# Optimization experiments

Hardware: AMD Instinct MI355X
Metric: run time of the kernel (lower is better)

Reference implementation:

```python
import jax, jax.numpy as jnp
import numpy as np

# constants mirroring init_kwargs
SPATIAL_STRIDE = 4
RADIUS2 = 0.5 ** 2
K = 32


def _fps(xyz, m):
    """Iterative farthest point sampling. xyz: [N,3] -> idx [m] int32 (starts at index 0, like pointnet2)."""
    n = xyz.shape[0]

    def body(i, carry):
        dist, idx = carry
        cur = xyz[idx[i]]                              # [3]
        d = jnp.sum((xyz - cur) ** 2, axis=-1)          # [N]
        dist = jnp.minimum(dist, d)
        idx = idx.at[i + 1].set(jnp.argmax(dist).astype(jnp.int32))
        return dist, idx

    dist0 = jnp.full((n,), 1e10, xyz.dtype)
    idx0 = jnp.zeros((m,), jnp.int32)
    _, idx = jax.lax.fori_loop(0, m - 1, body, (dist0, idx0))
    return idx


def setup_inputs() -> dict:
    key = jax.random.key(0)
    ks = jax.random.split(key, 5)
    B, T, N, C = 4, 8, 2048, 64
    C_IN = 2 * C + 3  # grouped feat2 + anchor feat1 + xyz displacement
    xyzs = jax.random.uniform(ks[0], (B, T, N, 3), dtype=jnp.float32)
    features = jax.random.normal(ks[1], (B, T, N, C), dtype=jnp.float32)
    w1 = jax.random.normal(ks[2], (C_IN, 128), dtype=jnp.float32) / np.sqrt(C_IN)
    w2 = jax.random.normal(ks[3], (128, 128), dtype=jnp.float32) / np.sqrt(128)
    w3 = jax.random.normal(ks[4], (128, 256), dtype=jnp.float32) / np.sqrt(128)
    return {
        "xyzs": xyzs, "features": features,
        "w1": w1, "b1": jnp.zeros((128,), jnp.float32),
        "w2": w2, "b2": jnp.zeros((128,), jnp.float32),
        "w3": w3, "b3": jnp.zeros((256,), jnp.float32),
    }


def reference(xyzs, features, w1, b1, w2, b2, w3, b3):
    B, T, N, _ = xyzs.shape
    M = N // SPATIAL_STRIDE

    # temporal replicate padding [1,1]
    xp = jnp.concatenate([xyzs[:, :1], xyzs, xyzs[:, -1:]], axis=1)        # [B,T+2,N,3]
    fp = jnp.concatenate([features[:, :1], features, features[:, -1:]], axis=1)
    # frames processed: i = 1..T (stride 1); neighbor frame = i+1
    xyz_a, xyz_n = xp[:, 1:T + 1], xp[:, 2:T + 2]                          # [B,T,N,3]
    feat_a, feat_n = fp[:, 1:T + 1], fp[:, 2:T + 2]                        # [B,T,N,C]

    gather = jax.vmap(jax.vmap(lambda a, i: a[i]))  # over (B, T)

    # FPS on each anchor frame
    idx = jax.vmap(jax.vmap(lambda p: _fps(p, M)))(xyz_a)                  # [B,T,M]
    anchor = gather(xyz_a, idx)                                            # [B,T,M,3]
    f1 = gather(feat_a, idx)                                               # [B,T,M,C]

    # knn of anchors into next frame, with ball-query radius clamp
    d = jnp.sum((anchor[:, :, :, None, :] - xyz_n[:, :, None, :, :]) ** 2, axis=-1)  # [B,T,M,N]
    negd, idxk = jax.lax.top_k(-d, K)                                      # [B,T,M,K]
    idxk = jnp.where(-negd <= RADIUS2, idxk, idxk[..., :1])                # duplicate nearest outside radius

    gxyz = gather(xyz_n, idxk)                                             # [B,T,M,K,3]
    gf2 = gather(feat_n, idxk)                                             # [B,T,M,K,C]
    disp = gxyz - anchor[:, :, :, None, :]
    h = jnp.concatenate(
        [gf2, jnp.broadcast_to(f1[:, :, :, None, :], gf2.shape), disp], axis=-1)  # [B,T,M,K,2C+3]

    h = jax.nn.relu(h @ w1 + b1)
    h = jax.nn.relu(h @ w2 + b2)
    h = jax.nn.relu(h @ w3 + b3)
    new_features = jnp.max(h, axis=3)                                      # [B,T,M,256]
    return anchor, new_features
```

## Files before the change

### kernel.cpp

```cpp
#include <hip/hip_runtime.h>

#define BB 4
#define TT 8
#define NN 2048
#define CC 64
#define MM 512
#define KK 32
#define H3DIM 256
#define RAD2 0.25f
#define FINF 3.4e38f

typedef _Float16 f16x8 __attribute__((ext_vector_type(8)));
typedef _Float16 f16x4 __attribute__((ext_vector_type(4)));
typedef float f32x4 __attribute__((ext_vector_type(4)));

template <int CTRL>
__device__ __forceinline__ float dpp_max_step(float x) {
    int xi = __builtin_bit_cast(int, x);
    int yi = __builtin_amdgcn_update_dpp(xi, xi, CTRL, 0xf, 0xf, false);
    return fmaxf(x, __builtin_bit_cast(float, yi));
}
__device__ __forceinline__ float wave_max64(float x) {
    x = dpp_max_step<0x111>(x);
    x = dpp_max_step<0x112>(x);
    x = dpp_max_step<0x114>(x);
    x = dpp_max_step<0x118>(x);
    x = dpp_max_step<0x142>(x);
    x = dpp_max_step<0x143>(x);
    return __builtin_bit_cast(float, __builtin_amdgcn_readlane(__builtin_bit_cast(int, x), 63));
}
template <int CTRL>
__device__ __forceinline__ float dpp_min_step(float x) {
    int xi = __builtin_bit_cast(int, x);
    int yi = __builtin_amdgcn_update_dpp(xi, xi, CTRL, 0xf, 0xf, false);
    return fminf(x, __builtin_bit_cast(float, yi));
}
__device__ __forceinline__ float wave_minf64(float x) {
    x = dpp_min_step<0x111>(x);
    x = dpp_min_step<0x112>(x);
    x = dpp_min_step<0x114>(x);
    x = dpp_min_step<0x118>(x);
    x = dpp_min_step<0x142>(x);
    x = dpp_min_step<0x143>(x);
    return __builtin_bit_cast(float, __builtin_amdgcn_readlane(__builtin_bit_cast(int, x), 63));
}
template <int CTRL>
__device__ __forceinline__ int dpp_imin_step(int x) {
    int yi = __builtin_amdgcn_update_dpp(x, x, CTRL, 0xf, 0xf, false);
    return (yi < x) ? yi : x;
}
__device__ __forceinline__ int wave_mini64(int x) {
    x = dpp_imin_step<0x111>(x);
    x = dpp_imin_step<0x112>(x);
    x = dpp_imin_step<0x114>(x);
    x = dpp_imin_step<0x118>(x);
    x = dpp_imin_step<0x142>(x);
    x = dpp_imin_step<0x143>(x);
    return __builtin_amdgcn_readlane(x, 63);
}

__global__ __launch_bounds__(256) void k_fps(const float* __restrict__ xyzs,
                                             int* __restrict__ fps_idx) {
    int bt = blockIdx.x;
    int tid = threadIdx.x;
    int lane = tid & 63, w = tid >> 6;
    __shared__ float sx[NN], sy[NN], sz[NN];
    __shared__ float pd[2][4];
    __shared__ int   pi[2][4];
    const float* src = xyzs + (size_t)bt * NN * 3;
    for (int i = tid; i < NN; i += 256) {
        sx[i] = src[i * 3 + 0];
        sy[i] = src[i * 3 + 1];
        sz[i] = src[i * 3 + 2];
    }
    __syncthreads();

    float px[8], py[8], pz[8], dist[8];
#pragma unroll
    for (int j = 0; j < 8; ++j) {
        int p = tid * 8 + j;
        px[j] = sx[p]; py[j] = sy[p]; pz[j] = sz[p];
        dist[j] = 1e10f;
    }

    int cur = 0;
    if (tid == 0) fps_idx[bt * MM + 0] = 0;
    int pbase = tid * 8;

    for (int it = 1; it < MM; ++it) {
        float cx = sx[cur], cy = sy[cur], cz = sz[cur];
        float bestd = -1.0f;
        int bestp = 0;
#pragma unroll
        for (int j = 0; j < 8; ++j) {
            float dx = px[j] - cx, dy = py[j] - cy, dz = pz[j] - cz;
            float d = dx * dx + dy * dy + dz * dz;
            float nd = fminf(dist[j], d);
            dist[j] = nd;
            if (nd > bestd) { bestd = nd; bestp = pbase + j; }
        }
        float wmax = wave_max64(bestd);
        unsigned long long mask = __ballot(bestd == wmax);
        int wl = __ffsll(mask) - 1;
        int wbp = __builtin_amdgcn_readlane(bestp, wl);
        if (lane == 0) { pd[it & 1][w] = wmax; pi[it & 1][w] = wbp; }
        __syncthreads();
        float bd = pd[it & 1][0];
        int bp = pi[it & 1][0];
#pragma unroll
        for (int q = 1; q < 4; ++q) {
            float d2 = pd[it & 1][q];
            int p2 = pi[it & 1][q];
            if (d2 > bd) { bd = d2; bp = p2; }
        }
        cur = bp;
        if (tid == 0) fps_idx[bt * MM + it] = cur;
    }
}

__global__ __launch_bounds__(256) void k_pp(const float* __restrict__ xyzs,
                                            const float* __restrict__ feats,
                                            const float* __restrict__ w1,
                                            _Float16* __restrict__ Pp) {
    __shared__ float sw[68 * 128];
    __shared__ float sin_[64 * 68];
    int tid = threadIdx.x;
    for (int i = tid; i < 68 * 128; i += 256) {
        int r = i >> 7, c = i & 127;
        float v = 0.f;
        if (r < 64) v = w1[r * 128 + c];
        else if (r < 67) v = w1[(128 + r - 64) * 128 + c];
        sw[i] = v;
    }
    int row0 = blockIdx.x * 64;
    int bt = row0 >> 11;
    int b = bt >> 3, t = bt & 7;
    int tn = (t + 1 < TT) ? (t + 1) : (TT - 1);
    size_t nbase = (size_t)(b * TT + tn) * NN + (row0 & (NN - 1));
    const float* fsrc = feats + nbase * CC;
    const float* xsrc = xyzs + nbase * 3;
    for (int i = tid; i < 1024; i += 256) {
        float4 v = ((const float4*)fsrc)[i];
        int r = i >> 4, c = (i & 15) * 4;
        *(float4*)&sin_[r * 68 + c] = v;
    }
    if (tid < 192) {
        int r = tid / 3, c = tid - r * 3;
        sin_[r * 68 + 64 + c] = xsrc[tid];
    }
    if (tid < 64) sin_[tid * 68 + 67] = 0.f;
    __syncthreads();

    int rowg = tid >> 5, colg = tid & 31;
    float4 acc[8];
#pragma unroll
    for (int i = 0; i < 8; ++i) acc[i] = make_float4(0.f, 0.f, 0.f, 0.f);
    for (int k = 0; k < 68; k += 4) {
        float4 a4[8], b4[4];
#pragma unroll
        for (int i = 0; i < 8; ++i) a4[i] = *(const float4*)&sin_[(rowg * 8 + i) * 68 + k];
#pragma unroll
        for (int kk = 0; kk < 4; ++kk) b4[kk] = *(const float4*)&sw[(k + kk) * 128 + colg * 4];
#pragma unroll
        for (int i = 0; i < 8; ++i) {
#pragma unroll
            for (int kk = 0; kk < 4; ++kk) {
                float av = (kk == 0) ? a4[i].x : (kk == 1) ? a4[i].y : (kk == 2) ? a4[i].z : a4[i].w;
                acc[i].x += av * b4[kk].x;
                acc[i].y += av * b4[kk].y;
                acc[i].z += av * b4[kk].z;
                acc[i].w += av * b4[kk].w;
            }
        }
    }
#pragma unroll
    for (int i = 0; i < 8; ++i) {
        f16x4 h;
        h[0] = (_Float16)acc[i].x; h[1] = (_Float16)acc[i].y;
        h[2] = (_Float16)acc[i].z; h[3] = (_Float16)acc[i].w;
        *(f16x4*)&Pp[(size_t)(row0 + rowg * 8 + i) * 128 + colg * 4] = h;
    }
}

__global__ __launch_bounds__(256) void k_qp(const float* __restrict__ xyzs,
                                            const float* __restrict__ feats,
                                            const float* __restrict__ w1,
                                            const float* __restrict__ b1,
                                            const int* __restrict__ fps_idx,
                                            float* __restrict__ Qp,
                                            float* __restrict__ out_anchor) {
    __shared__ float sw[68 * 128];
    __shared__ float sin_[64 * 68];
    __shared__ float sb[128];
    int tid = threadIdx.x;
    for (int i = tid; i < 68 * 128; i += 256) {
        int r = i >> 7, c = i & 127;
        float v = 0.f;
        if (r < 64) v = w1[(64 + r) * 128 + c];
        else if (r < 67) v = w1[(128 + r - 64) * 128 + c];
        sw[i] = v;
    }
    if (tid < 128) sb[tid] = b1[tid];
    int row0 = blockIdx.x * 64;
    int bt = row0 >> 9;
    size_t fbase = (size_t)bt * NN;
    {
        int r = tid >> 2, seg = tid & 3;
        int aidx = fps_idx[row0 + r];
        const float4* fr = (const float4*)(feats + (fbase + aidx) * CC);
#pragma unroll
        for (int i = 0; i < 4; ++i) {
            float4 v = fr[seg * 4 + i];
            *(float4*)&sin_[r * 68 + seg * 16 + i * 4] = v;
        }
    }
    if (tid < 64) {
        int aidx = fps_idx[row0 + tid];
        const float* xs = xyzs + (fbase + aidx) * 3;
        float x = xs[0], y = xs[1], z = xs[2];
        sin_[tid * 68 + 64] = -x;
        sin_[tid * 68 + 65] = -y;
        sin_[tid * 68 + 66] = -z;
        sin_[tid * 68 + 67] = 0.f;
        out_anchor[(size_t)(row0 + tid) * 3 + 0] = x;
        out_anchor[(size_t)(row0 + tid) * 3 + 1] = y;
        out_anchor[(size_t)(row0 + tid) * 3 + 2] = z;
    }
    __syncthreads();

    int rowg = tid >> 5, colg = tid & 31;
    float4 bias = *(const float4*)&sb[colg * 4];
    float4 acc[8];
#pragma unroll
    for (int i = 0; i < 8; ++i) acc[i] = bias;
    for (int k = 0; k < 68; k += 4) {
        float4 a4[8], b4[4];
#pragma unroll
        for (int i = 0; i < 8; ++i) a4[i] = *(const float4*)&sin_[(rowg * 8 + i) * 68 + k];
#pragma unroll
        for (int kk = 0; kk < 4; ++kk) b4[kk] = *(const float4*)&sw[(k + kk) * 128 + colg * 4];
#pragma unroll
        for (int i = 0; i < 8; ++i) {
#pragma unroll
            for (int kk = 0; kk < 4; ++kk) {
                float av = (kk == 0) ? a4[i].x : (kk == 1) ? a4[i].y : (kk == 2) ? a4[i].z : a4[i].w;
                acc[i].x += av * b4[kk].x;
                acc[i].y += av * b4[kk].y;
                acc[i].z += av * b4[kk].z;
                acc[i].w += av * b4[kk].w;
            }
        }
    }
#pragma unroll
    for (int i = 0; i < 8; ++i)
        *(float4*)&Qp[(size_t)(row0 + rowg * 8 + i) * 128 + colg * 4] = acc[i];
}

__global__ __launch_bounds__(256) void k_knn(const float* __restrict__ xyzs,
                                             const float* __restrict__ anchors,
                                             int* __restrict__ idxk) {
    __shared__ float sx[NN], sy[NN], sz[NN];
    int tid = threadIdx.x;
    int wave = tid >> 6, lane = tid & 63;
    int bt = blockIdx.x >> 6;
    int sub = blockIdx.x & 63;
    int b = bt >> 3, t = bt & 7;
    int tn = (t + 1 < TT) ? (t + 1) : (TT - 1);
    const float* src = xyzs + ((size_t)(b * TT + tn)) * NN * 3;
    for (int i = tid; i < NN; i += 256) {
        sx[i] = src[i * 3 + 0];
        sy[i] = src[i * 3 + 1];
        sz[i] = src[i * 3 + 2];
    }
    __syncthreads();

    for (int a = 0; a < 2; ++a) {
        int mrow = bt * MM + sub * 8 + wave * 2 + a;
        float ax = anchors[mrow * 3 + 0];
        float ay = anchors[mrow * 3 + 1];
        float az = anchors[mrow * 3 + 2];
        float d[32];
#pragma unroll
        for (int j = 0; j < 32; ++j) {
            int p = j * 64 + lane;
            float dx = sx[p] - ax, dy = sy[p] - ay, dz = sz[p] - az;
            d[j] = dx * dx + dy * dy + dz * dz;
        }
        float bd = FINF;
        int bp = 0x7fffffff;
#pragma unroll
        for (int j = 0; j < 32; ++j) {
            if (d[j] < bd) { bd = d[j]; bp = j * 64 + lane; }
        }
        float wmin = wave_minf64(bd);
        int cand = (bd == wmin) ? bp : 0x7fffffff;
        int gp = wave_mini64(cand);
        int p0 = gp;
        int myidx = gp;
        int pstar = gp;

        for (int r = 1; r < KK; ++r) {
            bd = FINF;
            bp = 0x7fffffff;
#pragma unroll
            for (int j = 0; j < 32; ++j) {
                int pj = j * 64 + lane;
                float dj = (pj == pstar) ? FINF : d[j];
                d[j] = dj;
                if (dj < bd) { bd = dj; bp = pj; }
            }
            wmin = wave_minf64(bd);
            cand = (bd == wmin) ? bp : 0x7fffffff;
            gp = wave_mini64(cand);
            int outp = (wmin <= RAD2) ? gp : p0;
            if (lane == r) myidx = outp;
            pstar = gp;
        }
        if (lane < KK) idxk[(size_t)mrow * KK + lane] = myidx;
    }
}

#define SM_W2 0
#define SM_W3 32768
#define SM_H1 98304
#define SM_H2 114688
#define SM_B2 131072
#define SM_B3 131584
#define SM_TOTAL 132608

__global__ __launch_bounds__(512, 1) void k_mlp(const _Float16* __restrict__ Pp,
                                                const float* __restrict__ Qp,
                                                const int* __restrict__ idxk,
                                                const float* __restrict__ w2,
                                                const float* __restrict__ b2,
                                                const float* __restrict__ w3,
                                                const float* __restrict__ b3,
                                                float* __restrict__ out_feat) {
    extern __shared__ char smem[];
    int tid = threadIdx.x;
    int bid = blockIdx.x;

    for (int i = tid; i < 128 * 128; i += 512) {
        int n = i & 127, kk = i >> 7;
        _Float16 v = (_Float16)w2[kk * 128 + n];
        *(_Float16*)(smem + SM_W2 + n * 256 + ((2 * kk) ^ ((n & 7) << 4))) = v;
    }
    for (int i = tid; i < 256 * 128; i += 512) {
        int n = i & 255, kk = i >> 8;
        _Float16 v = (_Float16)w3[kk * 256 + n];
        *(_Float16*)(smem + SM_W3 + n * 256 + ((2 * kk) ^ ((n & 7) << 4))) = v;
    }
    if (tid < 128) *(float*)(smem + SM_B2 + tid * 4) = b2[tid];
    if (tid < 256) *(float*)(smem + SM_B3 + tid * 4) = b3[tid];
    __syncthreads();

    int lane = tid & 63;
    int w = tid >> 6;
    int wm = w >> 2, wn = w & 3;
    int l15 = lane & 15, g = lane >> 4;
    int hswz = (l15 & 7) << 4;

    const f32x4 zero4 = {0.f, 0.f, 0.f, 0.f};

    for (int c = 0; c < 32; ++c) {
        int a0 = bid * 64 + c * 2;
        int bt = a0 >> 9;

        {
            int r = tid >> 3, seg = tid & 7;
            int arow = a0 + (r >> 5);
            int kidx = r & 31;
            int nk = idxk[(size_t)arow * KK + kidx];
            const _Float16* ps = Pp + ((size_t)(bt * NN + nk)) * 128 + seg * 16;
            const float* qs = Qp + (size_t)arow * 128 + seg * 16;
            int rowbase = SM_H1 + r * 256;
            int swz = (r & 7) << 4;
#pragma unroll
            for (int i = 0; i < 2; ++i) {
                f16x8 pv = *(const f16x8*)(ps + i * 8);
                f32x4 q0 = *(const f32x4*)(qs + i * 8);
                f32x4 q1 = *(const f32x4*)(qs + i * 8 + 4);
                f16x8 hv;
#pragma unroll
                for (int j = 0; j < 4; ++j) hv[j] = (_Float16)fmaxf((float)pv[j] + q0[j], 0.f);
#pragma unroll
                for (int j = 0; j < 4; ++j) hv[4 + j] = (_Float16)fmaxf((float)pv[4 + j] + q1[j], 0.f);
                *(f16x8*)(smem + rowbase + ((seg * 32 + i * 16) ^ swz)) = hv;
            }
        }
        __syncthreads();

        f32x4 acc2[2][2];
#pragma unroll
        for (int m = 0; m < 2; ++m)
#pragma unroll
            for (int n = 0; n < 2; ++n) acc2[m][n] = zero4;

#pragma unroll
        for (int ks = 0; ks < 4; ++ks) {
            int kbyte = ks * 64 + g * 16;
            f16x8 af[2], bf[2];
#pragma unroll
            for (int m = 0; m < 2; ++m) {
                int row = wm * 32 + m * 16 + l15;
                af[m] = *(const f16x8*)(smem + SM_H1 + row * 256 + (kbyte ^ hswz));
            }
#pragma unroll
            for (int n = 0; n < 2; ++n) {
                int col = wn * 32 + n * 16 + l15;
                bf[n] = *(const f16x8*)(smem + SM_W2 + col * 256 + (kbyte ^ hswz));
            }
#pragma unroll
            for (int m = 0; m < 2; ++m)
#pragma unroll
                for (int n = 0; n < 2; ++n)
                    acc2[m][n] = __builtin_amdgcn_mfma_f32_16x16x32_f16(af[m], bf[n], acc2[m][n], 0, 0, 0);
        }
#pragma unroll
        for (int m = 0; m < 2; ++m)
#pragma unroll
            for (int n = 0; n < 2; ++n) {
                int col = wn * 32 + n * 16 + l15;
                float bb = *(const float*)(smem + SM_B2 + col * 4);
#pragma unroll
                for (int r = 0; r < 4; ++r) {
                    int row = wm * 32 + m * 16 + g * 4 + r;
                    float v = fmaxf(acc2[m][n][r] + bb, 0.f);
                    *(_Float16*)(smem + SM_H2 + row * 256 + ((2 * col) ^ ((row & 7) << 4))) = (_Float16)v;
                }
            }
        __syncthreads();

        f32x4 acc3[2][4];
#pragma unroll
        for (int m = 0; m < 2; ++m)
#pragma unroll
            for (int n = 0; n < 4; ++n) acc3[m][n] = zero4;

#pragma unroll
        for (int ks = 0; ks < 4; ++ks) {
            int kbyte = ks * 64 + g * 16;
            f16x8 af[2], bf[4];
#pragma unroll
            for (int m = 0; m < 2; ++m) {
                int row = wm * 32 + m * 16 + l15;
                af[m] = *(const f16x8*)(smem + SM_H2 + row * 256 + (kbyte ^ hswz));
            }
#pragma unroll
            for (int n = 0; n < 4; ++n) {
                int col = wn * 64 + n * 16 + l15;
                bf[n] = *(const f16x8*)(smem + SM_W3 + col * 256 + (kbyte ^ hswz));
            }
#pragma unroll
            for (int m = 0; m < 2; ++m)
#pragma unroll
                for (int n = 0; n < 4; ++n)
                    acc3[m][n] = __builtin_amdgcn_mfma_f32_16x16x32_f16(af[m], bf[n], acc3[m][n], 0, 0, 0);
        }
#pragma unroll
        for (int n = 0; n < 4; ++n) {
            int col = wn * 64 + n * 16 + l15;
            float s = acc3[0][n][0];
#pragma unroll
            for (int r = 1; r < 4; ++r) s = fmaxf(s, acc3[0][n][r]);
#pragma unroll
            for (int r = 0; r < 4; ++r) s = fmaxf(s, acc3[1][n][r]);
            s = fmaxf(s, __shfl_xor(s, 16));
            s = fmaxf(s, __shfl_xor(s, 32));
            if (g == 0) {
                float bb = *(const float*)(smem + SM_B3 + col * 4);
                out_feat[(size_t)(a0 + wm) * H3DIM + col] = fmaxf(s + bb, 0.f);
            }
        }
        __syncthreads();
    }
}

extern "C" void kernel_launch(void* const* d_in, const int* in_sizes, int n_in,
                              void* d_out, int out_size, void* d_ws, size_t ws_size,
                              hipStream_t stream) {
    const float* xyzs  = (const float*)d_in[0];
    const float* feats = (const float*)d_in[1];
    const float* w1 = (const float*)d_in[2];
    const float* b1 = (const float*)d_in[3];
    const float* w2 = (const float*)d_in[4];
    const float* b2 = (const float*)d_in[5];
    const float* w3 = (const float*)d_in[6];
    const float* b3 = (const float*)d_in[7];

    float* out_anchor = (float*)d_out;
    float* out_feat = out_anchor + (size_t)BB * TT * MM * 3;

    char* ws = (char*)d_ws;
    int* fps_idx = (int*)ws;
    int* idxk = (int*)(ws + 65536);
    _Float16* Pp = (_Float16*)(ws + 65536 + 2097152);
    float* Qp = (float*)(ws + 65536 + 2097152 + 16777216);
    if (ws_size < (size_t)(65536 + 2097152 + 16777216) + (size_t)BB * TT * MM * 128 * 4)
        return;

    k_fps<<<BB * TT, 256, 0, stream>>>(xyzs, fps_idx);
    k_pp<<<BB * TT * NN / 64, 256, 0, stream>>>(xyzs, feats, w1, Pp);
    k_qp<<<BB * TT * MM / 64, 256, 0, stream>>>(xyzs, feats, w1, b1, fps_idx, Qp, out_anchor);
    k_knn<<<BB * TT * 64, 256, 0, stream>>>(xyzs, out_anchor, idxk);

    (void)hipFuncSetAttribute((const void*)k_mlp, hipFuncAttributeMaxDynamicSharedMemorySize, SM_TOTAL);
    k_mlp<<<256, 512, SM_TOTAL, stream>>>(Pp, Qp, idxk, w2, b2, w3, b3, out_feat);
}
```

Before: 595.8 us.

## Pack distance and index into 64-bit keys for single-pass wave argmax/argmin

FPS and kNN reductions now pack the float distance and point index into one 64-bit key, so a single DPP reduction finds both the extreme value and the winning index. This replaces the separate max, ballot and readlane sequence, or the min-value then min-index pair of reductions. In FPS the winning wave writes the winner's coordinates into shared memory alongside the key, which removes the dependent LDS read of the next centroid on the serial critical path. In kNN the per-lane scan becomes a tree of four groups, and only the winning lane's slot is invalidated, which shortens the dependency chain. The cost is that each DPP step moves two 32-bit halves and does a 64-bit compare; tie-breaking relies on the non-negative float bit patterns ordering the same way as the floats.

```diff
diff --git a/kernel.cpp b/kernel.cpp
--- a/kernel.cpp
+++ b/kernel.cpp
@@ -15,58 +15,53 @@
 typedef float f32x4 __attribute__((ext_vector_type(4)));
 
 template <int CTRL>
-__device__ __forceinline__ float dpp_max_step(float x) {
-    int xi = __builtin_bit_cast(int, x);
-    int yi = __builtin_amdgcn_update_dpp(xi, xi, CTRL, 0xf, 0xf, false);
-    return fmaxf(x, __builtin_bit_cast(float, yi));
-}
-__device__ __forceinline__ float wave_max64(float x) {
-    x = dpp_max_step<0x111>(x);
-    x = dpp_max_step<0x112>(x);
-    x = dpp_max_step<0x114>(x);
-    x = dpp_max_step<0x118>(x);
-    x = dpp_max_step<0x142>(x);
-    x = dpp_max_step<0x143>(x);
-    return __builtin_bit_cast(float, __builtin_amdgcn_readlane(__builtin_bit_cast(int, x), 63));
+__device__ __forceinline__ unsigned long long dpp_maxkey_step(unsigned long long k) {
+    int lo = (int)(unsigned)k;
+    int hi = (int)(unsigned)(k >> 32);
+    int slo = __builtin_amdgcn_update_dpp(lo, lo, CTRL, 0xf, 0xf, false);
+    int shi = __builtin_amdgcn_update_dpp(hi, hi, CTRL, 0xf, 0xf, false);
+    unsigned long long s = ((unsigned long long)(unsigned)shi << 32) | (unsigned)slo;
+    return s > k ? s : k;
 }
 template <int CTRL>
-__device__ __forceinline__ float dpp_min_step(float x) {
-    int xi = __builtin_bit_cast(int, x);
-    int yi = __builtin_amdgcn_update_dpp(xi, xi, CTRL, 0xf, 0xf, false);
-    return fminf(x, __builtin_bit_cast(float, yi));
-}
-__device__ __forceinline__ float wave_minf64(float x) {
-    x = dpp_min_step<0x111>(x);
-    x = dpp_min_step<0x112>(x);
-    x = dpp_min_step<0x114>(x);
-    x = dpp_min_step<0x118>(x);
-    x = dpp_min_step<0x142>(x);
-    x = dpp_min_step<0x143>(x);
-    return __builtin_bit_cast(float, __builtin_amdgcn_readlane(__builtin_bit_cast(int, x), 63));
-}
-template <int CTRL>
-__device__ __forceinline__ int dpp_imin_step(int x) {
-    int yi = __builtin_amdgcn_update_dpp(x, x, CTRL, 0xf, 0xf, false);
-    return (yi < x) ? yi : x;
-}
-__device__ __forceinline__ int wave_mini64(int x) {
-    x = dpp_imin_step<0x111>(x);
-    x = dpp_imin_step<0x112>(x);
-    x = dpp_imin_step<0x114>(x);
-    x = dpp_imin_step<0x118>(x);
-    x = dpp_imin_step<0x142>(x);
-    x = dpp_imin_step<0x143>(x);
-    return __builtin_amdgcn_readlane(x, 63);
+__device__ __forceinline__ unsigned long long dpp_minkey_step(unsigned long long k) {
+    int lo = (int)(unsigned)k;
+    int hi = (int)(unsigned)(k >> 32);
+    int slo = __builtin_amdgcn_update_dpp(lo, lo, CTRL, 0xf, 0xf, false);
+    int shi = __builtin_amdgcn_update_dpp(hi, hi, CTRL, 0xf, 0xf, false);
+    unsigned long long s = ((unsigned long long)(unsigned)shi << 32) | (unsigned)slo;
+    return s < k ? s : k;
+}
+__device__ __forceinline__ unsigned long long wave_maxkey(unsigned long long k) {
+    k = dpp_maxkey_step<0x111>(k);
+    k = dpp_maxkey_step<0x112>(k);
+    k = dpp_maxkey_step<0x114>(k);
+    k = dpp_maxkey_step<0x118>(k);
+    k = dpp_maxkey_step<0x142>(k);
+    k = dpp_maxkey_step<0x143>(k);
+    int lo = __builtin_amdgcn_readlane((int)(unsigned)k, 63);
+    int hi = __builtin_amdgcn_readlane((int)(unsigned)(k >> 32), 63);
+    return ((unsigned long long)(unsigned)hi << 32) | (unsigned)lo;
+}
+__device__ __forceinline__ unsigned long long wave_minkey(unsigned long long k) {
+    k = dpp_minkey_step<0x111>(k);
+    k = dpp_minkey_step<0x112>(k);
+    k = dpp_minkey_step<0x114>(k);
+    k = dpp_minkey_step<0x118>(k);
+    k = dpp_minkey_step<0x142>(k);
+    k = dpp_minkey_step<0x143>(k);
+    int lo = __builtin_amdgcn_readlane((int)(unsigned)k, 63);
+    int hi = __builtin_amdgcn_readlane((int)(unsigned)(k >> 32), 63);
+    return ((unsigned long long)(unsigned)hi << 32) | (unsigned)lo;
 }
 
 __global__ __launch_bounds__(256) void k_fps(const float* __restrict__ xyzs,
                                              int* __restrict__ fps_idx) {
     int bt = blockIdx.x;
     int tid = threadIdx.x;
-    int lane = tid & 63, w = tid >> 6;
+    int w = tid >> 6;
     __shared__ float sx[NN], sy[NN], sz[NN];
-    __shared__ float pd[2][4];
-    __shared__ int   pi[2][4];
+    __shared__ int recs[2][4][8];
     const float* src = xyzs + (size_t)bt * NN * 3;
     for (int i = tid; i < NN; i += 256) {
         sx[i] = src[i * 3 + 0];
@@ -83,12 +78,11 @@
         dist[j] = 1e10f;
     }
 
-    int cur = 0;
     if (tid == 0) fps_idx[bt * MM + 0] = 0;
     int pbase = tid * 8;
+    float cx = sx[0], cy = sy[0], cz = sz[0];
 
     for (int it = 1; it < MM; ++it) {
-        float cx = sx[cur], cy = sy[cur], cz = sz[cur];
         float bestd = -1.0f;
         int bestp = 0;
 #pragma unroll
@@ -99,22 +93,59 @@
             dist[j] = nd;
             if (nd > bestd) { bestd = nd; bestp = pbase + j; }
         }
-        float wmax = wave_max64(bestd);
-        unsigned long long mask = __ballot(bestd == wmax);
-        int wl = __ffsll(mask) - 1;
-        int wbp = __builtin_amdgcn_readlane(bestp, wl);
-        if (lane == 0) { pd[it & 1][w] = wmax; pi[it & 1][w] = wbp; }
+        unsigned long long mykey =
+            ((unsigned long long)(unsigned)__builtin_bit_cast(unsigned, bestd) << 32) |
+            (unsigned)(~(unsigned)bestp);
+        unsigned long long wkey = wave_maxkey(mykey);
+        if (mykey == wkey) {
+            int j3 = bestp & 7;
+            bool b0 = (j3 & 1) != 0, b1 = (j3 & 2) != 0, b2 = (j3 & 4) != 0;
+            float x01 = b0 ? px[1] : px[0], x23 = b0 ? px[3] : px[2];
+            float x45 = b0 ? px[5] : px[4], x67 = b0 ? px[7] : px[6];
+            float y01 = b0 ? py[1] : py[0], y23 = b0 ? py[3] : py[2];
+            float y45 = b0 ? py[5] : py[4], y67 = b0 ? py[7] : py[6];
+            float z01 = b0 ? pz[1] : pz[0], z23 = b0 ? pz[3] : pz[2];
+            float z45 = b0 ? pz[5] : pz[4], z67 = b0 ? pz[7] : pz[6];
+            float x0123 = b1 ? x23 : x01, x4567 = b1 ? x67 : x45;
+            float y0123 = b1 ? y23 : y01, y4567 = b1 ? y67 : y45;
+            float z0123 = b1 ? z23 : z01, z4567 = b1 ? z67 : z45;
+            float wx = b2 ? x4567 : x0123;
+            float wy = b2 ? y4567 : y0123;
+            float wz = b2 ? z4567 : z0123;
+            int* rec = &recs[it & 1][w][0];
+            rec[0] = (int)(unsigned)(wkey >> 32);
+            rec[1] = (int)(unsigned)wkey;
+            rec[2] = __builtin_bit_cast(int, wx);
+            rec[3] = __builtin_bit_cast(int, wy);
+            rec[4] = __builtin_bit_cast(int, wz);
+        }
         __syncthreads();
-        float bd = pd[it & 1][0];
-        int bp = pi[it & 1][0];
-#pragma unroll
-        for (int q = 1; q < 4; ++q) {
-            float d2 = pd[it & 1][q];
-            int p2 = pi[it & 1][q];
-            if (d2 > bd) { bd = d2; bp = p2; }
-        }
-        cur = bp;
-        if (tid == 0) fps_idx[bt * MM + it] = cur;
+        int4 r0 = *(const int4*)&recs[it & 1][0][0];
+        float z0 = __builtin_bit_cast(float, recs[it & 1][0][4]);
+        int4 r1 = *(const int4*)&recs[it & 1][1][0];
+        float z1 = __builtin_bit_cast(float, recs[it & 1][1][4]);
+        int4 r2 = *(const int4*)&recs[it & 1][2][0];
+        float z2 = __builtin_bit_cast(float, recs[it & 1][2][4]);
+        int4 r3 = *(const int4*)&recs[it & 1][3][0];
+        float z3 = __builtin_bit_cast(float, recs[it & 1][3][4]);
+        unsigned long long k0 = ((unsigned long long)(unsigned)r0.x << 32) | (unsigned)r0.y;
+        unsigned long long k1 = ((unsigned long long)(unsigned)r1.x << 32) | (unsigned)r1.y;
+        unsigned long long k2 = ((unsigned long long)(unsigned)r2.x << 32) | (unsigned)r2.y;
+        unsigned long long k3 = ((unsigned long long)(unsigned)r3.x << 32) | (unsigned)r3.y;
+        bool t01 = k1 > k0, t23 = k3 > k2;
+        unsigned long long ka = t01 ? k1 : k0, kb = t23 ? k3 : k2;
+        float xa = __builtin_bit_cast(float, t01 ? r1.z : r0.z);
+        float ya = __builtin_bit_cast(float, t01 ? r1.w : r0.w);
+        float za = t01 ? z1 : z0;
+        float xb = __builtin_bit_cast(float, t23 ? r3.z : r2.z);
+        float yb = __builtin_bit_cast(float, t23 ? r3.w : r2.w);
+        float zb = t23 ? z3 : z2;
+        bool tf = kb > ka;
+        unsigned long long kf = tf ? kb : ka;
+        cx = tf ? xb : xa;
+        cy = tf ? yb : ya;
+        cz = tf ? zb : za;
+        if (tid == 0) fps_idx[bt * MM + it] = (int)(~(unsigned)kf);
     }
 }
 
@@ -286,35 +317,44 @@
             float dx = sx[p] - ax, dy = sy[p] - ay, dz = sz[p] - az;
             d[j] = dx * dx + dy * dy + dz * dz;
         }
-        float bd = FINF;
-        int bp = 0x7fffffff;
-#pragma unroll
-        for (int j = 0; j < 32; ++j) {
-            if (d[j] < bd) { bd = d[j]; bp = j * 64 + lane; }
-        }
-        float wmin = wave_minf64(bd);
-        int cand = (bd == wmin) ? bp : 0x7fffffff;
-        int gp = wave_mini64(cand);
-        int p0 = gp;
-        int myidx = gp;
-        int pstar = gp;
-
-        for (int r = 1; r < KK; ++r) {
-            bd = FINF;
-            bp = 0x7fffffff;
-#pragma unroll
-            for (int j = 0; j < 32; ++j) {
-                int pj = j * 64 + lane;
-                float dj = (pj == pstar) ? FINF : d[j];
-                d[j] = dj;
-                if (dj < bd) { bd = dj; bp = pj; }
-            }
-            wmin = wave_minf64(bd);
-            cand = (bd == wmin) ? bp : 0x7fffffff;
-            gp = wave_mini64(cand);
-            int outp = (wmin <= RAD2) ? gp : p0;
+        int p0 = 0;
+        int myidx = 0;
+        for (int r = 0; r < KK; ++r) {
+            float gd[4];
+            int gp[4];
+#pragma unroll
+            for (int g = 0; g < 4; ++g) {
+                gd[g] = d[g * 8];
+                gp[g] = (g * 8) * 64 + lane;
+#pragma unroll
+                for (int jj = 1; jj < 8; ++jj) {
+                    float dj = d[g * 8 + jj];
+                    if (dj < gd[g]) { gd[g] = dj; gp[g] = (g * 8 + jj) * 64 + lane; }
+                }
+            }
+            bool u01 = gd[1] < gd[0], u23 = gd[3] < gd[2];
+            float da = u01 ? gd[1] : gd[0], db = u23 ? gd[3] : gd[2];
+            int pa = u01 ? gp[1] : gp[0], pb = u23 ? gp[3] : gp[2];
+            bool uf = db < da;
+            float bd = uf ? db : da;
+            int bp = uf ? pb : pa;
+            unsigned long long key =
+                ((unsigned long long)(unsigned)__builtin_bit_cast(unsigned, bd) << 32) |
+                (unsigned)bp;
+            unsigned long long wkey = wave_minkey(key);
+            int pstar = (int)(unsigned)wkey;
+            float dstar = __builtin_bit_cast(float, (unsigned)(wkey >> 32));
+            if (r == 0) { p0 = pstar; myidx = pstar; }
+            int outp = (dstar <= RAD2) ? pstar : p0;
             if (lane == r) myidx = outp;
-            pstar = gp;
+            if (r < KK - 1) {
+                int lanew = pstar & 63;
+                int jw = pstar >> 6;
+                bool imw = (lane == lanew);
+#pragma unroll
+                for (int j = 0; j < 32; ++j)
+                    d[j] = (imw && j == jw) ? FINF : d[j];
+            }
         }
         if (lane < KK) idxk[(size_t)mrow * KK + lane] = myidx;
     }
```

After: 632.1 us. 1.06x slower.
